# Kernel tuning notes

Hardware: AMD Instinct MI355X
Metric: run time of the kernel (lower is better)

The kernel has to match this reference:

```python
import jax, jax.numpy as jnp
import numpy as np

B, C, H, W = 16, 64, 128, 128
K = 3  # dynamic kernel size


def setup_inputs() -> dict:
    key = jax.random.key(0)
    ks = jax.random.split(key, 6)
    return {
        "x": jax.random.normal(ks[0], (B, C, H, W), jnp.float32),       # feature map
        "d": jax.random.normal(ks[1], (B, 64), jnp.float32),            # degradation repr
        "Wk1": jax.random.normal(ks[2], (64, 64), jnp.float32) * 0.05,  # Linear(64,64), no bias
        "Wk2": jax.random.normal(ks[3], (64 * K * K, 64), jnp.float32) * 0.05,  # Linear(64,576)
        "Wc": jax.random.normal(ks[4], (64, 64), jnp.float32) * 0.05,   # 1x1 conv weight (out,in)
        "bc": jnp.zeros((64,), jnp.float32),                            # 1x1 conv bias
    }


def _lrelu(v):
    return jnp.where(v >= 0, v, 0.1 * v)


def reference(x, d, Wk1, Wk2, Wc, bc):
    b, c, h, w = x.shape
    k = K
    # kernel-generating MLP: Linear -> LeakyReLU(0.1) -> Linear
    hid = _lrelu(d @ Wk1.T)                      # (B, 64)
    kern = (hid @ Wk2.T).reshape(b, c, 1, k, k)   # one 3x3 kernel per (batch, channel)

    # dynamic depthwise 3x3 conv: per-sample kernels, groups == channels
    def dwconv(xi, ki):
        # xi: (C,H,W), ki: (C,1,3,3) in OIHW with feature_group_count=C
        return jax.lax.conv_general_dilated(
            xi[None], ki, window_strides=(1, 1), padding='SAME',
            feature_group_count=c,
            dimension_numbers=('NCHW', 'OIHW', 'NCHW'))[0]

    out = jax.vmap(dwconv)(x, kern)              # (B,C,H,W)
    out = _lrelu(out)
    # 1x1 pointwise conv with bias
    out = jnp.einsum('bchw,oc->bohw', out, Wc) + bc[None, :, None, None]
    return out
```

## Files before the change

### kernel.cpp

```cpp
#include <hip/hip_runtime.h>

#define Bn 16
#define Cn 64
#define Hn 128
#define Wn 128
#define HWn (Hn * Wn)

typedef __attribute__((ext_vector_type(8)))  short  short8;
typedef __attribute__((ext_vector_type(16))) float  floatx16;
typedef __attribute__((ext_vector_type(4)))  float  floatx4;
using int32x4 = int __attribute__((ext_vector_type(4)));

__device__ floatx4
llvm_amdgcn_raw_buffer_load_v4f32(int32x4 srsrc, int voffset, int soffset,
                                  int aux) __asm("llvm.amdgcn.raw.buffer.load.v4f32");

__device__ __forceinline__ int32x4 make_rsrc(const void* p, int bytes) {
    int32x4 r;
    r.x = (int)(unsigned)(uintptr_t)p;
    r.y = (int)((uintptr_t)p >> 32);
    r.z = bytes;
    r.w = 0x00020000;
    return r;
}

__device__ __forceinline__ unsigned short f2bf(float f) {
    unsigned u = __float_as_uint(f);
    u += 0x7fffu + ((u >> 16) & 1u);
    return (unsigned short)(u >> 16);
}
__device__ __forceinline__ float lrelu(float v) { return v >= 0.f ? v : 0.1f * v; }

#define SYNC_LDS() asm volatile("s_waitcnt lgkmcnt(0)\n\ts_barrier" ::: "memory")

__global__ __launch_bounds__(192)
void gen_kern7(const float* __restrict__ d,
               const float* __restrict__ Wk1,
               const float* __restrict__ Wk2,
               const float* __restrict__ Wc,
               float* __restrict__ kernP,
               unsigned short* __restrict__ WcT) {
    const int b = blockIdx.x;
    const int r = blockIdx.y;
    const int t = threadIdx.x;
    __shared__ float hid_s[64];

    if (t < 64) {
        const float4* __restrict__ w4 = (const float4*)(Wk1 + (size_t)t * 64);
        const float*  __restrict__ db = d + b * 64;
        float s0 = 0.f, s1 = 0.f, s2 = 0.f, s3 = 0.f;
        #pragma unroll
        for (int j = 0; j < 16; ++j) {
            const float4 wv = w4[j];
            s0 += db[4 * j + 0] * wv.x;
            s1 += db[4 * j + 1] * wv.y;
            s2 += db[4 * j + 2] * wv.z;
            s3 += db[4 * j + 3] * wv.w;
        }
        hid_s[t] = lrelu((s0 + s1) + (s2 + s3));
    }
    __syncthreads();

    {
        const int o = r * 192 + t;
        const float4* __restrict__ w4 = (const float4*)(Wk2 + (size_t)o * 64);
        const float4* __restrict__ h4 = (const float4*)hid_s;
        float s0 = 0.f, s1 = 0.f, s2 = 0.f, s3 = 0.f;
        #pragma unroll
        for (int j = 0; j < 16; ++j) {
            const float4 wv = w4[j];
            const float4 hv = h4[j];
            s0 += hv.x * wv.x;
            s1 += hv.y * wv.y;
            s2 += hv.z * wv.z;
            s3 += hv.w * wv.w;
        }
        const int c = o / 9, tap = o - c * 9;
        kernP[b * 768 + c * 12 + tap] = (s0 + s1) + (s2 + s3);
    }

    if (b == 0 && r == 0) {
        for (int idx = t; idx < 4096; idx += 192) {
            const int j    = idx & 7;
            const int lane = (idx >> 3) & 63;
            const int g    = (idx >> 9) & 3;
            const int m    = idx >> 11;
            const int col  = lane & 31, kh = lane >> 5;
            const int o    = m * 32 + col;
            const int c    = g * 16 + kh * 8 + j;
            WcT[idx] = f2bf(Wc[o * 64 + c]);
        }
    }
}

struct XK { floatx4 x[3][2]; };
struct KF { floatx4 k0, k1; float k8; };

__device__ __forceinline__ void issue_x(XK& v, int32x4 rs, int c,
                                        const int* rofsB, int px0) {
    #pragma unroll
    for (int r = 0; r < 3; ++r) {
        const int vo = (c << 16) + rofsB[r] + px0 * 4;
        v.x[r][0] = llvm_amdgcn_raw_buffer_load_v4f32(rs, vo, 0, 0);
        v.x[r][1] = llvm_amdgcn_raw_buffer_load_v4f32(rs, vo + 16, 0, 0);
    }
}

__device__ __forceinline__ void issue_k(KF& kf, const float* kp, int c) {
    const floatx4* k4 = (const floatx4*)(kp + c * 12);
    kf.k0 = k4[0];
    kf.k1 = k4[1];
    kf.k8 = ((const float*)k4)[8];
}

__device__ __forceinline__ short8 compute_dw(const XK& v, const KF& kf,
                                             int lane, int tm) {
    float t0[8], t1[8], t2[8];
    #pragma unroll
    for (int i = 0; i < 8; ++i) {
        const float xr0 = (i < 4) ? v.x[0][0][i] : v.x[0][1][i - 4];
        const float xr1 = (i < 4) ? v.x[1][0][i] : v.x[1][1][i - 4];
        const float xr2 = (i < 4) ? v.x[2][0][i] : v.x[2][1][i - 4];
        t0[i] = kf.k0.x * xr0 + kf.k0.w * xr1 + kf.k1.z * xr2;
        t1[i] = kf.k0.y * xr0 + kf.k1.x * xr1 + kf.k1.w * xr2;
        t2[i] = kf.k0.z * xr0 + kf.k1.y * xr1 + kf.k8   * xr2;
    }
    float t0m = __shfl(t0[7], lane - 1, 64);
    float t2p = __shfl(t2[0], lane + 1, 64);
    if (tm == 0)  t0m = 0.f;
    if (tm == 15) t2p = 0.f;

    float dw[8];
    dw[0] = t0m + t1[0] + t2[1];
    #pragma unroll
    for (int i = 1; i < 7; ++i) dw[i] = t0[i - 1] + t1[i] + t2[i + 1];
    dw[7] = t0[6] + t1[7] + t2p;

    short8 w8;
    #pragma unroll
    for (int i = 0; i < 8; ++i) w8[i] = (short)f2bf(lrelu(dw[i]));
    return w8;
}

__global__ __launch_bounds__(256, 4)
void da_mfma5(const float* __restrict__ x,
              const float* __restrict__ kernP,
              const unsigned short* __restrict__ WcT,
              const float* __restrict__ bc,
              float* __restrict__ out) {
    const int t    = threadIdx.x;
    const int lane = t & 63;
    const int wv   = t >> 6;
    const int col  = lane & 31;
    const int kh   = lane >> 5;
    const int bx   = blockIdx.x;
    const int h    = ((bx & 7) << 4) | (bx >> 3);
    const int b    = blockIdx.y;
    const int px   = wv * 32 + col;

    const int sch = t >> 4;
    const int tm  = t & 15;
    const int px0 = tm * 8;

    __shared__ unsigned short dwB[2][2048];

    int rofsB[3];
    #pragma unroll
    for (int i = 0; i < 3; ++i) {
        const int hh = h + i - 1;
        rofsB[i] = (hh >= 0 && hh < Hn) ? hh * (Wn * 4) : 0x10000000;
    }

    const int32x4 rs = make_rsrc(x + (size_t)b * Cn * HWn, Cn * HWn * 4);
    const float* __restrict__ kp = kernP + b * 768;

    floatx16 acc[2];
    #pragma unroll
    for (int m = 0; m < 2; ++m)
        #pragma unroll
        for (int r = 0; r < 16; ++r)
            acc[m][r] = 0.f;

    XK X[4]; KF Kf[4]; short8 a0[4], a1[4];
    a0[0] = *(const short8*)(WcT + ((0 * 4 + 0) * 64 + lane) * 8);
    a1[0] = *(const short8*)(WcT + ((1 * 4 + 0) * 64 + lane) * 8);
    issue_k(Kf[0], kp, sch);
    issue_k(Kf[1], kp, 16 + sch);
    issue_x(X[0], rs, sch, rofsB, px0);
    issue_x(X[1], rs, 16 + sch, rofsB, px0);
    {
        const short8 w8 = compute_dw(X[0], Kf[0], lane, tm);
        *(short8*)&dwB[0][sch * 128 + (px0 ^ ((sch & 8) << 2))] = w8;
    }
    SYNC_LDS();

    #pragma unroll
    for (int g = 0; g < 4; ++g) {
        if (g < 2) issue_x(X[g + 2], rs, (g + 2) * 16 + sch, rofsB, px0);
        if (g < 3) {
            a0[g + 1] = *(const short8*)(WcT + ((0 * 4 + g + 1) * 64 + lane) * 8);
            a1[g + 1] = *(const short8*)(WcT + ((1 * 4 + g + 1) * 64 + lane) * 8);
        }
        if (g < 2) issue_k(Kf[g + 2], kp, (g + 2) * 16 + sch);

        short8 bfr;
        #pragma unroll
        for (int j = 0; j < 8; ++j) {
            const int cl = kh * 8 + j;
            bfr[j] = (short)dwB[g & 1][cl * 128 + (px ^ ((cl & 8) << 2))];
        }
        acc[0] = __builtin_amdgcn_mfma_f32_32x32x16_bf16(a0[g], bfr, acc[0], 0, 0, 0);
        acc[1] = __builtin_amdgcn_mfma_f32_32x32x16_bf16(a1[g], bfr, acc[1], 0, 0, 0);

        if (g < 3) {
            const short8 w8 = compute_dw(X[g + 1], Kf[g + 1], lane, tm);
            *(short8*)&dwB[(g + 1) & 1][sch * 128 + (px0 ^ ((sch & 8) << 2))] = w8;
            SYNC_LDS();
        }
    }

    float* __restrict__ ob = out + (size_t)b * Cn * HWn + h * Wn + px;
    #pragma unroll
    for (int m = 0; m < 2; ++m)
        #pragma unroll
        for (int q = 0; q < 4; ++q) {
            const float4 bv = *(const float4*)&bc[m * 32 + q * 8 + 4 * kh];
            #pragma unroll
            for (int j = 0; j < 4; ++j) {
                const int o = m * 32 + q * 8 + 4 * kh + j;
                ob[(size_t)o * HWn] = acc[m][q * 4 + j] + ((const float*)&bv)[j];
            }
        }
}

extern "C" void kernel_launch(void* const* d_in, const int* in_sizes, int n_in,
                              void* d_out, int out_size, void* d_ws, size_t ws_size,
                              hipStream_t stream) {
    const float* x   = (const float*)d_in[0];
    const float* d   = (const float*)d_in[1];
    const float* Wk1 = (const float*)d_in[2];
    const float* Wk2 = (const float*)d_in[3];
    const float* Wc  = (const float*)d_in[4];
    const float* bc  = (const float*)d_in[5];
    float* out = (float*)d_out;
    float*          kernP = (float*)d_ws;
    unsigned short* WcT   = (unsigned short*)((float*)d_ws + Bn * 768);

    gen_kern7<<<dim3(Bn, 3), dim3(192), 0, stream>>>(d, Wk1, Wk2, Wc, kernP, WcT);
    da_mfma5<<<dim3(Hn, Bn), dim3(256), 0, stream>>>(x, kernP, WcT, bc, out);
}
```

Baseline: 137.7 us.

## Process four output rows per block to reuse halo rows of x

Each block now computes four consecutive image rows instead of one, loading six input rows per channel group rather than three per row. This cuts redundant reads of the vertical halo rows from about three times to one and a half, and reuses the kernel taps and Wc fragments across four rows. The cost is many more accumulator registers (eight 16-wide accumulators), which is why launch bounds drop to two blocks per SM. The grid also shrinks to a quarter of the blocks, and the previous software pipelining across channel groups is simplified.

New measurement: 133.2 us. 1.03x faster.

```diff
diff --git a/kernel.cpp b/kernel.cpp
--- a/kernel.cpp
+++ b/kernel.cpp
@@ -93,57 +93,10 @@
     }
 }
 
-struct XK { floatx4 x[3][2]; };
 struct KF { floatx4 k0, k1; float k8; };
 
-__device__ __forceinline__ void issue_x(XK& v, int32x4 rs, int c,
-                                        const int* rofsB, int px0) {
-    #pragma unroll
-    for (int r = 0; r < 3; ++r) {
-        const int vo = (c << 16) + rofsB[r] + px0 * 4;
-        v.x[r][0] = llvm_amdgcn_raw_buffer_load_v4f32(rs, vo, 0, 0);
-        v.x[r][1] = llvm_amdgcn_raw_buffer_load_v4f32(rs, vo + 16, 0, 0);
-    }
-}
-
-__device__ __forceinline__ void issue_k(KF& kf, const float* kp, int c) {
-    const floatx4* k4 = (const floatx4*)(kp + c * 12);
-    kf.k0 = k4[0];
-    kf.k1 = k4[1];
-    kf.k8 = ((const float*)k4)[8];
-}
-
-__device__ __forceinline__ short8 compute_dw(const XK& v, const KF& kf,
-                                             int lane, int tm) {
-    float t0[8], t1[8], t2[8];
-    #pragma unroll
-    for (int i = 0; i < 8; ++i) {
-        const float xr0 = (i < 4) ? v.x[0][0][i] : v.x[0][1][i - 4];
-        const float xr1 = (i < 4) ? v.x[1][0][i] : v.x[1][1][i - 4];
-        const float xr2 = (i < 4) ? v.x[2][0][i] : v.x[2][1][i - 4];
-        t0[i] = kf.k0.x * xr0 + kf.k0.w * xr1 + kf.k1.z * xr2;
-        t1[i] = kf.k0.y * xr0 + kf.k1.x * xr1 + kf.k1.w * xr2;
-        t2[i] = kf.k0.z * xr0 + kf.k1.y * xr1 + kf.k8   * xr2;
-    }
-    float t0m = __shfl(t0[7], lane - 1, 64);
-    float t2p = __shfl(t2[0], lane + 1, 64);
-    if (tm == 0)  t0m = 0.f;
-    if (tm == 15) t2p = 0.f;
-
-    float dw[8];
-    dw[0] = t0m + t1[0] + t2[1];
-    #pragma unroll
-    for (int i = 1; i < 7; ++i) dw[i] = t0[i - 1] + t1[i] + t2[i + 1];
-    dw[7] = t0[6] + t1[7] + t2p;
-
-    short8 w8;
-    #pragma unroll
-    for (int i = 0; i < 8; ++i) w8[i] = (short)f2bf(lrelu(dw[i]));
-    return w8;
-}
-
-__global__ __launch_bounds__(256, 4)
-void da_mfma5(const float* __restrict__ x,
+__global__ __launch_bounds__(256, 2)
+void da_mfma9(const float* __restrict__ x,
               const float* __restrict__ kernP,
               const unsigned short* __restrict__ WcT,
               const float* __restrict__ bc,
@@ -153,73 +106,108 @@
     const int wv   = t >> 6;
     const int col  = lane & 31;
     const int kh   = lane >> 5;
-    const int bx   = blockIdx.x;
-    const int h    = ((bx & 7) << 4) | (bx >> 3);
+    const int hbl  = blockIdx.x;
+    const int hb   = ((hbl & 7) << 2) | (hbl >> 3);
+    const int h0   = hb * 4;
     const int b    = blockIdx.y;
     const int px   = wv * 32 + col;
 
     const int sch = t >> 4;
-    const int tm  = t & 15;
-    const int px0 = tm * 8;
-
-    __shared__ unsigned short dwB[2][2048];
-
-    int rofsB[3];
-    #pragma unroll
-    for (int i = 0; i < 3; ++i) {
-        const int hh = h + i - 1;
-        rofsB[i] = (hh >= 0 && hh < Hn) ? hh * (Wn * 4) : 0x10000000;
+    const int oct = t & 15;
+    const int px0 = oct * 8;
+
+    __shared__ unsigned short dwS[2][4][16][128];
+
+    int rofs[6];
+    #pragma unroll
+    for (int i = 0; i < 6; ++i) {
+        const int hr = h0 + i - 1;
+        rofs[i] = (hr >= 0 && hr < Hn) ? hr * (Wn * 4) : 0x10000000;
     }
 
     const int32x4 rs = make_rsrc(x + (size_t)b * Cn * HWn, Cn * HWn * 4);
     const float* __restrict__ kp = kernP + b * 768;
 
-    floatx16 acc[2];
-    #pragma unroll
-    for (int m = 0; m < 2; ++m)
-        #pragma unroll
-        for (int r = 0; r < 16; ++r)
-            acc[m][r] = 0.f;
-
-    XK X[4]; KF Kf[4]; short8 a0[4], a1[4];
-    a0[0] = *(const short8*)(WcT + ((0 * 4 + 0) * 64 + lane) * 8);
-    a1[0] = *(const short8*)(WcT + ((1 * 4 + 0) * 64 + lane) * 8);
-    issue_k(Kf[0], kp, sch);
-    issue_k(Kf[1], kp, 16 + sch);
-    issue_x(X[0], rs, sch, rofsB, px0);
-    issue_x(X[1], rs, 16 + sch, rofsB, px0);
-    {
-        const short8 w8 = compute_dw(X[0], Kf[0], lane, tm);
-        *(short8*)&dwB[0][sch * 128 + (px0 ^ ((sch & 8) << 2))] = w8;
-    }
-    SYNC_LDS();
+    floatx16 acc[4][2];
+    #pragma unroll
+    for (int r = 0; r < 4; ++r)
+        #pragma unroll
+        for (int m = 0; m < 2; ++m)
+            #pragma unroll
+            for (int e = 0; e < 16; ++e)
+                acc[r][m][e] = 0.f;
+
+    floatx4 X[6][2];
+    #define LOAD_X(G)                                                        \
+        _Pragma("unroll")                                                    \
+        for (int i = 0; i < 6; ++i) {                                        \
+            const int vo = (((G) * 16 + sch) << 16) + rofs[i] + px0 * 4;     \
+            X[i][0] = llvm_amdgcn_raw_buffer_load_v4f32(rs, vo, 0, 0);       \
+            X[i][1] = llvm_amdgcn_raw_buffer_load_v4f32(rs, vo + 16, 0, 0);  \
+        }
+
+    LOAD_X(0);
 
     #pragma unroll
     for (int g = 0; g < 4; ++g) {
-        if (g < 2) issue_x(X[g + 2], rs, (g + 2) * 16 + sch, rofsB, px0);
-        if (g < 3) {
-            a0[g + 1] = *(const short8*)(WcT + ((0 * 4 + g + 1) * 64 + lane) * 8);
-            a1[g + 1] = *(const short8*)(WcT + ((1 * 4 + g + 1) * 64 + lane) * 8);
-        }
-        if (g < 2) issue_k(Kf[g + 2], kp, (g + 2) * 16 + sch);
-
-        short8 bfr;
-        #pragma unroll
-        for (int j = 0; j < 8; ++j) {
-            const int cl = kh * 8 + j;
-            bfr[j] = (short)dwB[g & 1][cl * 128 + (px ^ ((cl & 8) << 2))];
-        }
-        acc[0] = __builtin_amdgcn_mfma_f32_32x32x16_bf16(a0[g], bfr, acc[0], 0, 0, 0);
-        acc[1] = __builtin_amdgcn_mfma_f32_32x32x16_bf16(a1[g], bfr, acc[1], 0, 0, 0);
-
-        if (g < 3) {
-            const short8 w8 = compute_dw(X[g + 1], Kf[g + 1], lane, tm);
-            *(short8*)&dwB[(g + 1) & 1][sch * 128 + (px0 ^ ((sch & 8) << 2))] = w8;
-            SYNC_LDS();
-        }
-    }
-
-    float* __restrict__ ob = out + (size_t)b * Cn * HWn + h * Wn + px;
+        const int buf = g & 1;
+        KF kf;
+        {
+            const floatx4* k4 = (const floatx4*)(kp + (g * 16 + sch) * 12);
+            kf.k0 = k4[0];
+            kf.k1 = k4[1];
+            kf.k8 = ((const float*)k4)[8];
+        }
+
+        #pragma unroll
+        for (int rr = 0; rr < 4; ++rr) {
+            float t0[8], t1[8], t2[8];
+            #pragma unroll
+            for (int i = 0; i < 8; ++i) {
+                const float xr0 = (i < 4) ? X[rr][0][i]     : X[rr][1][i - 4];
+                const float xr1 = (i < 4) ? X[rr + 1][0][i] : X[rr + 1][1][i - 4];
+                const float xr2 = (i < 4) ? X[rr + 2][0][i] : X[rr + 2][1][i - 4];
+                t0[i] = kf.k0.x * xr0 + kf.k0.w * xr1 + kf.k1.z * xr2;
+                t1[i] = kf.k0.y * xr0 + kf.k1.x * xr1 + kf.k1.w * xr2;
+                t2[i] = kf.k0.z * xr0 + kf.k1.y * xr1 + kf.k8   * xr2;
+            }
+            float t0m = __shfl(t0[7], lane - 1, 64);
+            float t2p = __shfl(t2[0], lane + 1, 64);
+            if (oct == 0)  t0m = 0.f;
+            if (oct == 15) t2p = 0.f;
+
+            float dw[8];
+            dw[0] = t0m + t1[0] + t2[1];
+            #pragma unroll
+            for (int i = 1; i < 7; ++i) dw[i] = t0[i - 1] + t1[i] + t2[i + 1];
+            dw[7] = t0[6] + t1[7] + t2p;
+
+            short8 w8;
+            #pragma unroll
+            for (int i = 0; i < 8; ++i) w8[i] = (short)f2bf(lrelu(dw[i]));
+            *(short8*)&dwS[buf][rr][sch][px0 ^ ((sch & 8) << 2)] = w8;
+        }
+
+        if (g < 3) { LOAD_X(g + 1); }
+
+        SYNC_LDS();
+
+        const short8 a0 = *(const short8*)(WcT + ((0 * 4 + g) * 64 + lane) * 8);
+        const short8 a1 = *(const short8*)(WcT + ((1 * 4 + g) * 64 + lane) * 8);
+        #pragma unroll
+        for (int rr = 0; rr < 4; ++rr) {
+            short8 bfr;
+            #pragma unroll
+            for (int j = 0; j < 8; ++j) {
+                const int cl = kh * 8 + j;
+                bfr[j] = (short)dwS[buf][rr][cl][px ^ ((cl & 8) << 2)];
+            }
+            acc[rr][0] = __builtin_amdgcn_mfma_f32_32x32x16_bf16(a0, bfr, acc[rr][0], 0, 0, 0);
+            acc[rr][1] = __builtin_amdgcn_mfma_f32_32x32x16_bf16(a1, bfr, acc[rr][1], 0, 0, 0);
+        }
+    }
+
+    float* __restrict__ ob = out + (size_t)b * Cn * HWn + (size_t)h0 * Wn + px;
     #pragma unroll
     for (int m = 0; m < 2; ++m)
         #pragma unroll
@@ -228,9 +216,12 @@
             #pragma unroll
             for (int j = 0; j < 4; ++j) {
                 const int o = m * 32 + q * 8 + 4 * kh + j;
-                ob[(size_t)o * HWn] = acc[m][q * 4 + j] + ((const float*)&bv)[j];
+                #pragma unroll
+                for (int r = 0; r < 4; ++r)
+                    ob[(size_t)o * HWn + r * Wn] = acc[r][m][q * 4 + j] + ((const float*)&bv)[j];
             }
         }
+    #undef LOAD_X
 }
 
 extern "C" void kernel_launch(void* const* d_in, const int* in_sizes, int n_in,
@@ -247,5 +238,5 @@
     unsigned short* WcT   = (unsigned short*)((float*)d_ws + Bn * 768);
 
     gen_kern7<<<dim3(Bn, 3), dim3(192), 0, stream>>>(d, Wk1, Wk2, Wc, kernP, WcT);
-    da_mfma5<<<dim3(Hn, Bn), dim3(256), 0, stream>>>(x, kernP, WcT, bc, out);
-}
+    da_mfma9<<<dim3(Hn / 4, Bn), dim3(256), 0, stream>>>(x, kernP, WcT, bc, out);
+}
```
